# Performance work log

Hardware: AMD Instinct MI355X
Metric: run time of the kernel (lower is better)

## Reference

```python
import jax, jax.numpy as jnp
import numpy as np

D_MODEL = 1024
NUM_HEADS = 16
D_HEAD = D_MODEL // NUM_HEADS
THETA = 10000.0
NEG_INF = -1e9


def apply_rope(x, theta=THETA):
    # x: (..., S, Dh) with interleaved pairs (2i, 2i+1)
    S, Dh = x.shape[-2], x.shape[-1]
    inv_freq = 1.0 / (theta ** (jnp.arange(0, Dh, 2, dtype=jnp.float32) / Dh))  # (Dh/2,)
    ang = jnp.arange(S, dtype=jnp.float32)[:, None] * inv_freq[None, :]          # (S, Dh/2)
    cos, sin = jnp.cos(ang), jnp.sin(ang)
    x1 = x[..., 0::2]
    x2 = x[..., 1::2]
    r1 = x1 * cos - x2 * sin
    r2 = x1 * sin + x2 * cos
    # interleave back
    return jnp.stack([r1, r2], axis=-1).reshape(x.shape)


def setup_inputs() -> dict:
    key = jax.random.key(0)
    ks = jax.random.split(key, 5)
    B, S = 2, 2048
    scale = 1.0 / np.sqrt(D_MODEL)
    return {
        "x": jax.random.normal(ks[0], (B, S, D_MODEL), dtype=jnp.float32),
        "Wq": jax.random.normal(ks[1], (D_MODEL, D_MODEL), dtype=jnp.float32) * scale,
        "Wk": jax.random.normal(ks[2], (D_MODEL, D_MODEL), dtype=jnp.float32) * scale,
        "Wv": jax.random.normal(ks[3], (D_MODEL, D_MODEL), dtype=jnp.float32) * scale,
        "Wo": jax.random.normal(ks[4], (D_MODEL, D_MODEL), dtype=jnp.float32) * scale,
    }


def reference(x, Wq, Wk, Wv, Wo):
    B, S, _ = x.shape
    def split_heads(t):
        return t.reshape(B, S, NUM_HEADS, D_HEAD).transpose(0, 2, 1, 3)  # (B,H,S,Dh)
    # nn.Linear(bias=False): y = x @ W.T
    Q = split_heads(x @ Wq.T)
    K = split_heads(x @ Wk.T)
    V = split_heads(x @ Wv.T)
    Q = apply_rope(Q)
    K = apply_rope(K)
    scale = 1.0 / jnp.sqrt(jnp.asarray(D_HEAD, dtype=x.dtype))
    scores = jnp.einsum("bhqd,bhkd->bhqk", Q, K) * scale  # (B,H,S,S)
    causal = jnp.tril(jnp.ones((S, S), dtype=bool))
    scores = jnp.where(causal, scores, NEG_INF)
    attn = jax.nn.softmax(scores, axis=-1)
    out = jnp.einsum("bhqk,bhkd->bhqd", attn, V)
    out = out.transpose(0, 2, 1, 3).reshape(B, S, D_MODEL)
    return out @ Wo.T
```

## Files before the change

### kernel.cpp

```cpp
#include <hip/hip_runtime.h>
#include <hip/hip_bf16.h>
#include <stdint.h>

typedef __attribute__((ext_vector_type(8))) short bf8;
typedef __attribute__((ext_vector_type(4))) float f4;

#define MFMA16(a, b, c) __builtin_amdgcn_mfma_f32_16x16x32_bf16((a), (b), (c), 0, 0, 0)

static __device__ __forceinline__ short f2b(float f) {
  uint32_t x = __float_as_uint(f);
  x += 0x7fffu + ((x >> 16) & 1u);
  return (short)(x >> 16);
}

static __device__ __forceinline__ uint32_t pk2(float a, float b) {
  return ((__float_as_uint(a) + 0x8000u) >> 16) |
         ((__float_as_uint(b) + 0x8000u) & 0xffff0000u);
}

static __device__ __forceinline__ void gload16(const short* g, void* l) {
  __builtin_amdgcn_global_load_lds(
      (const __attribute__((address_space(1))) void*)g,
      (__attribute__((address_space(3))) void*)l, 16, 0, 0);
}

__global__ void rope_kernel(float2* __restrict__ tab) {
  const int t = blockIdx.x * 256 + threadIdx.x;
  const int s = t >> 5, i = t & 31;
  const float inv = powf(10000.0f, -(float)i * (1.0f / 32.0f));
  const float ang = (float)s * inv;
  float sv, cv;
  sincosf(ang, &sv, &cv);
  tab[t] = make_float2(cv, sv);
}

__global__ void convert_kernel(const float* __restrict__ x,
                               const float* __restrict__ wq, const float* __restrict__ wk,
                               const float* __restrict__ wv, const float* __restrict__ wo,
                               short* __restrict__ xb, short* __restrict__ Wb) {
  const size_t i = ((size_t)blockIdx.x * 256 + threadIdx.x) * 8;
  const float* __restrict__ src;
  short* __restrict__ dst;
  if (i < 4194304u) {
    src = x + i;
    dst = xb + i;
  } else {
    const size_t j = i - 4194304u;
    const int z = (int)(j >> 20);
    const size_t o = j & 1048575u;
    src = (z == 0 ? wq : z == 1 ? wk : z == 2 ? wv : wo) + o;
    dst = Wb + j;
  }
  const float4 a = *(const float4*)src;
  const float4 b = *(const float4*)(src + 4);
  bf8 v;
  v[0] = f2b(a.x); v[1] = f2b(a.y); v[2] = f2b(a.z); v[3] = f2b(a.w);
  v[4] = f2b(b.x); v[5] = f2b(b.y); v[6] = f2b(b.z); v[7] = f2b(b.w);
  *(bf8*)dst = v;
}

template <int MODE>
__launch_bounds__(256, 2)
__global__ void gemm_kernel(const short* __restrict__ Ab, const short* __restrict__ Wb,
                            short* __restrict__ Qo, short* __restrict__ Ko,
                            short* __restrict__ VTo, float* __restrict__ Fo,
                            const float2* __restrict__ rope) {
  constexpr int K = 1024;
  const int bm = blockIdx.x, bn = blockIdx.y;
  const int z = (MODE == 0) ? blockIdx.z : 3;
  const short* __restrict__ Bb = Wb + ((size_t)z << 20);

  __shared__ short As[128 * 64];
  __shared__ short Bs[128 * 64];

  const int tid = threadIdx.x;
  const int lane = tid & 63;
  const int wave = tid >> 6;
  const int wr = wave >> 1, wc = wave & 1;
  const int lg = lane >> 4, lr = lane & 15;

  f4 acc[4][4];
#pragma unroll
  for (int i = 0; i < 4; i++)
#pragma unroll
    for (int j = 0; j < 4; j++) {
      acc[i][j][0] = 0.f; acc[i][j][1] = 0.f;
      acc[i][j][2] = 0.f; acc[i][j][3] = 0.f;
    }

  const int kc = tid & 7;
  const int srow = tid >> 3;
  const int kcs = (kc ^ (srow & 7)) * 8;
  char* const Asw = (char*)As + wave * 1024;
  char* const Bsw = (char*)Bs + wave * 1024;

  for (int k0 = 0; k0 < K; k0 += 64) {
#pragma unroll
    for (int i = 0; i < 4; i++) {
      const int row = srow + i * 32;
      gload16(Ab + (size_t)(bm * 128 + row) * K + k0 + kcs, Asw + i * 4096);
      gload16(Bb + (size_t)(bn * 128 + row) * K + k0 + kcs, Bsw + i * 4096);
    }
    __syncthreads();
#pragma unroll
    for (int kk = 0; kk < 2; kk++) {
      bf8 af[4], bb[4];
#pragma unroll
      for (int mi = 0; mi < 4; mi++) {
        const int row = wr * 64 + mi * 16 + lr;
        const int lb = (row * 128 + kk * 64 + lg * 16) ^ ((row & 7) << 4);
        af[mi] = *(const bf8*)((const char*)As + lb);
      }
#pragma unroll
      for (int ni = 0; ni < 4; ni++) {
        const int row = wc * 64 + ni * 16 + lr;
        const int lb = (row * 128 + kk * 64 + lg * 16) ^ ((row & 7) << 4);
        bb[ni] = *(const bf8*)((const char*)Bs + lb);
      }
#pragma unroll
      for (int mi = 0; mi < 4; mi++)
#pragma unroll
        for (int ni = 0; ni < 4; ni++)
          acc[mi][ni] = MFMA16(af[mi], bb[ni], acc[mi][ni]);
    }
    __syncthreads();
  }

  if (MODE == 1) {
#pragma unroll
    for (int mi = 0; mi < 4; mi++) {
      const int m0 = bm * 128 + wr * 64 + mi * 16 + lg * 4;
#pragma unroll
      for (int ni = 0; ni < 4; ni++) {
        const int n = bn * 128 + wc * 64 + ni * 16 + lr;
#pragma unroll
        for (int r = 0; r < 4; r++)
          Fo[(size_t)(m0 + r) * 1024 + n] = acc[mi][ni][r];
      }
    }
    return;
  }

  if (z == 2) {
#pragma unroll
    for (int mi = 0; mi < 4; mi++) {
      const int m0 = bm * 128 + wr * 64 + mi * 16 + lg * 4;
      const int b = m0 >> 11, s0 = m0 & 2047;
#pragma unroll
      for (int ni = 0; ni < 4; ni++) {
        const int n = bn * 128 + wc * 64 + ni * 16 + lr;
        ushort4 pk;
        pk.x = (unsigned short)f2b(acc[mi][ni][0]);
        pk.y = (unsigned short)f2b(acc[mi][ni][1]);
        pk.z = (unsigned short)f2b(acc[mi][ni][2]);
        pk.w = (unsigned short)f2b(acc[mi][ni][3]);
        *(ushort4*)(VTo + ((size_t)((b * 16 + (n >> 6)) * 64 + (n & 63))) * 2048 + s0) = pk;
      }
    }
  } else {
    short* __restrict__ Out = (z == 0) ? Qo : Ko;
    const float qscale = (z == 0) ? 0.18033688011112042f : 1.0f;
#pragma unroll
    for (int mi = 0; mi < 4; mi++) {
      const int m0 = bm * 128 + wr * 64 + mi * 16 + lg * 4;
      const int b = m0 >> 11, s0 = m0 & 2047;
#pragma unroll
      for (int ni = 0; ni < 4; ni++) {
        const int n = bn * 128 + wc * 64 + ni * 16 + lr;
        const int h = n >> 6, d = n & 63;
        const float sgn = (d & 1) ? 1.0f : -1.0f;
#pragma unroll
        for (int r = 0; r < 4; r++) {
          const float v = acc[mi][ni][r];
          const float p = __shfl_xor(v, 1);
          const float2 cs = rope[((s0 + r) << 5) + (d >> 1)];
          const float res = (v * cs.x + sgn * p * cs.y) * qscale;
          Out[((size_t)(b * 16 + h) * 2048 + (s0 + r)) * 64 + d] = f2b(res);
        }
      }
    }
  }
}

__launch_bounds__(256, 2)
__global__ void attn_kernel(const short* __restrict__ Qg, const short* __restrict__ Kg,
                            const short* __restrict__ Vg, short* __restrict__ AO) {
  const int S = 2048;
  const int id = blockIdx.x;
  const int xcd = id & 7, r = id >> 3;
  const int bh = xcd * 4 + (r & 3);
  const int i = r >> 2;
  const int tid = threadIdx.x;
  const int lane = tid & 63, wave = tid >> 6;
  const int lg = lane >> 4, lr = lane & 15;
  const short* __restrict__ Qp = Qg + (size_t)bh * S * 64;
  const short* __restrict__ Kp = Kg + (size_t)bh * S * 64;
  const short* __restrict__ Vp = Vg + (size_t)bh * 64 * S;

  __shared__ short KB[2][64 * 64];
  __shared__ short VB[2][64 * 64];
  __shared__ short PB[4][2][16 * 64];

  const int tL = 16 * wave + i;
  const int tH = 127 - tL;
  const int qbaseT[2] = {tH << 4, tL << 4};
  const int nkvT[2] = {(16 * tH + 79) >> 6, (16 * tL + 79) >> 6};
  const int blk_nkv = (2111 - 16 * i) >> 6;

  const int rsub = lane >> 3;
  const int chsw = ((lane & 7) ^ rsub) * 8;
  const int row0 = (2 * wave) * 8 + rsub;
  const int row1 = (2 * wave + 1) * 8 + rsub;
  char* const kd0 = (char*)nullptr;

#define STAGE_KV(buf, kvb_)                                                        \
  do {                                                                             \
    gload16(Kp + (size_t)((kvb_) + row0) * 64 + chsw, (char*)KB[buf] + (2 * wave) * 1024);     \
    gload16(Kp + (size_t)((kvb_) + row1) * 64 + chsw, (char*)KB[buf] + (2 * wave + 1) * 1024); \
    gload16(Vp + (size_t)row0 * 2048 + (kvb_) + chsw, (char*)VB[buf] + (2 * wave) * 1024);     \
    gload16(Vp + (size_t)row1 * 2048 + (kvb_) + chsw, (char*)VB[buf] + (2 * wave + 1) * 1024); \
  } while (0)

  bf8 qf[2][2];
#pragma unroll
  for (int tt = 0; tt < 2; tt++)
#pragma unroll
    for (int ks = 0; ks < 2; ks++)
      qf[tt][ks] = *(const bf8*)(Qp + (size_t)(qbaseT[tt] + lr) * 64 + ks * 32 + lg * 8);

  f4 o[2][4];
#pragma unroll
  for (int tt = 0; tt < 2; tt++)
#pragma unroll
    for (int dt = 0; dt < 4; dt++) {
      o[tt][dt][0] = 0.f; o[tt][dt][1] = 0.f; o[tt][dt][2] = 0.f; o[tt][dt][3] = 0.f;
    }
  float mrun[2] = {-1e30f, -1e30f};
  float lsum[2] = {0.f, 0.f};

  char* const PwT[2] = {(char*)&PB[wave][0][0], (char*)&PB[wave][1][0]};
  const int rowoff = lr * 128;
  const int sw = (lr & 7) << 4;

  STAGE_KV(0, 0);
  __syncthreads();

  for (int kb = 0; kb < blk_nkv; kb++) {
    const int kvb = kb * 64;
    const int cur = kb & 1;

    if (kb + 1 < blk_nkv) STAGE_KV(cur ^ 1, kvb + 64);

    if (kb < nkvT[0]) {
      const char* Kc = (const char*)KB[cur];
      const char* Vc = (const char*)VB[cur];

      bf8 kf[4][2];
#pragma unroll
      for (int nt = 0; nt < 4; nt++) {
        const int row = nt * 16 + lr;
        const int base = row * 128 + lg * 16;
        const int rsw = (row & 7) << 4;
        kf[nt][0] = *(const bf8*)(Kc + (base ^ rsw));
        kf[nt][1] = *(const bf8*)(Kc + ((base + 64) ^ rsw));
      }

      asm volatile("s_waitcnt lgkmcnt(0)" ::: "memory");

#pragma unroll
      for (int tt = 0; tt < 2; tt++) {
        if (kb < nkvT[tt]) {
          f4 st[4];
          __builtin_amdgcn_s_setprio(1);
#pragma unroll
          for (int nt = 0; nt < 4; nt++) {
            f4 c;
            c[0] = 0.f; c[1] = 0.f; c[2] = 0.f; c[3] = 0.f;
            c = MFMA16(kf[nt][0], qf[tt][0], c);
            c = MFMA16(kf[nt][1], qf[tt][1], c);
            st[nt] = c;
          }
          __builtin_amdgcn_s_setprio(0);

          if ((kvb + 63) > qbaseT[tt]) {
            const int q = qbaseT[tt] + lr;
#pragma unroll
            for (int nt = 0; nt < 4; nt++)
#pragma unroll
              for (int rr = 0; rr < 4; rr++) {
                const int kv = kvb + nt * 16 + lg * 4 + rr;
                if (kv > q) st[nt][rr] = -1e9f;
              }
          }

          float m0 = fmaxf(fmaxf(st[0][0], st[0][1]), fmaxf(st[0][2], st[0][3]));
#pragma unroll
          for (int nt = 1; nt < 4; nt++)
            m0 = fmaxf(m0, fmaxf(fmaxf(st[nt][0], st[nt][1]), fmaxf(st[nt][2], st[nt][3])));
          m0 = fmaxf(m0, __shfl_xor(m0, 16));
          m0 = fmaxf(m0, __shfl_xor(m0, 32));

          if (__any(m0 - mrun[tt] > 8.0f)) {
            const float mn = fmaxf(mrun[tt], m0);
            const float corr = __builtin_amdgcn_exp2f(mrun[tt] - mn);
            mrun[tt] = mn;
            lsum[tt] *= corr;
#pragma unroll
            for (int rr = 0; rr < 4; rr++) {
              const float co = __shfl(corr, (lg << 2) + rr);
#pragma unroll
              for (int dt = 0; dt < 4; dt++) o[tt][dt][rr] *= co;
            }
          }

#pragma unroll
          for (int nt = 0; nt < 4; nt++) {
            const float p0 = __builtin_amdgcn_exp2f(st[nt][0] - mrun[tt]);
            const float p1 = __builtin_amdgcn_exp2f(st[nt][1] - mrun[tt]);
            const float p2 = __builtin_amdgcn_exp2f(st[nt][2] - mrun[tt]);
            const float p3 = __builtin_amdgcn_exp2f(st[nt][3] - mrun[tt]);
            lsum[tt] += (p0 + p1) + (p2 + p3);
            *(uint2*)(PwT[tt] + ((rowoff + nt * 32 + lg * 8) ^ sw)) =
                make_uint2(pk2(p0, p1), pk2(p2, p3));
          }
        }
      }

      asm volatile("s_waitcnt lgkmcnt(0)" ::: "memory");

      bf8 vf[4][2];
#pragma unroll
      for (int dt = 0; dt < 4; dt++) {
        const int row = dt * 16 + lr;
        const int base = row * 128 + lg * 16;
        const int rsw = (row & 7) << 4;
        vf[dt][0] = *(const bf8*)(Vc + (base ^ rsw));
        vf[dt][1] = *(const bf8*)(Vc + ((base + 64) ^ rsw));
      }

#pragma unroll
      for (int tt = 0; tt < 2; tt++) {
        if (kb < nkvT[tt]) {
          bf8 pf[2];
#pragma unroll
          for (int ks = 0; ks < 2; ks++)
            pf[ks] = *(const bf8*)(PwT[tt] + ((rowoff + ks * 64 + lg * 16) ^ sw));
          __builtin_amdgcn_s_setprio(1);
#pragma unroll
          for (int dt = 0; dt < 4; dt++) {
            o[tt][dt] = MFMA16(pf[0], vf[dt][0], o[tt][dt]);
            o[tt][dt] = MFMA16(pf[1], vf[dt][1], o[tt][dt]);
          }
          __builtin_amdgcn_s_setprio(0);
        }
      }
    }

    __syncthreads();
  }

  const int b = bh >> 4, h = bh & 15;
#pragma unroll
  for (int tt = 0; tt < 2; tt++) {
    float s = lsum[tt];
    s += __shfl_xor(s, 16);
    s += __shfl_xor(s, 32);
    const float inv = 1.0f / s;
    float inv_o[4];
#pragma unroll
    for (int rr = 0; rr < 4; rr++) inv_o[rr] = __shfl(inv, (lg << 2) + rr);
#pragma unroll
    for (int rr = 0; rr < 4; rr++) {
      const int q = qbaseT[tt] + lg * 4 + rr;
#pragma unroll
      for (int dt = 0; dt < 4; dt++) {
        const int d = dt * 16 + lr;
        AO[((size_t)b * 2048 + q) * 1024 + h * 64 + d] = f2b(o[tt][dt][rr] * inv_o[rr]);
      }
    }
  }
#undef STAGE_KV
}

extern "C" void kernel_launch(void* const* d_in, const int* in_sizes, int n_in,
                              void* d_out, int out_size, void* d_ws, size_t ws_size,
                              hipStream_t stream) {
  const float* x  = (const float*)d_in[0];
  const float* wq = (const float*)d_in[1];
  const float* wk = (const float*)d_in[2];
  const float* wv = (const float*)d_in[3];
  const float* wo = (const float*)d_in[4];
  float* out = (float*)d_out;

  char* ws = (char*)d_ws;
  short*  Qb  = (short*)(ws);
  short*  Kb  = (short*)(ws + (8ull  << 20));
  short*  VTb = (short*)(ws + (16ull << 20));
  short*  AOb = (short*)(ws + (24ull << 20));
  short*  xb  = AOb;
  short*  Wb  = (short*)(ws + (32ull << 20));
  float2* tab = (float2*)(ws + (40ull << 20));

  convert_kernel<<<4096, 256, 0, stream>>>(x, wq, wk, wv, wo, xb, Wb);
  rope_kernel<<<256, 256, 0, stream>>>(tab);
  gemm_kernel<0><<<dim3(32, 8, 3), 256, 0, stream>>>(
      xb, Wb, Qb, Kb, VTb, nullptr, tab);
  attn_kernel<<<512, 256, 0, stream>>>(Qb, Kb, VTb, AOb);
  gemm_kernel<1><<<dim3(32, 8, 1), 256, 0, stream>>>(
      AOb, Wb, nullptr, nullptr, nullptr, out, nullptr);
}
```

Measured before the change: 117.3 us.

## Split long causal query tiles across two KV segments and merge partial results

```diff
diff --git a/kernel.cpp b/kernel.cpp
--- a/kernel.cpp
+++ b/kernel.cpp
@@ -11,6 +11,10 @@
   uint32_t x = __float_as_uint(f);
   x += 0x7fffu + ((x >> 16) & 1u);
   return (short)(x >> 16);
+}
+
+static __device__ __forceinline__ float b2f(short v) {
+  return __uint_as_float(((uint32_t)(uint16_t)v) << 16);
 }
 
 static __device__ __forceinline__ uint32_t pk2(float a, float b) {
@@ -182,14 +186,19 @@
   }
 }
 
-__launch_bounds__(256, 2)
+__launch_bounds__(256, 4)
 __global__ void attn_kernel(const short* __restrict__ Qg, const short* __restrict__ Kg,
-                            const short* __restrict__ Vg, short* __restrict__ AO) {
+                            const short* __restrict__ Vg, short* __restrict__ AO,
+                            short* __restrict__ PO1, float* __restrict__ PM,
+                            float* __restrict__ PL) {
   const int S = 2048;
   const int id = blockIdx.x;
-  const int xcd = id & 7, r = id >> 3;
-  const int bh = xcd * 4 + (r & 3);
-  const int i = r >> 2;
+  const int xcd = id & 7;
+  const int rest = id >> 3;
+  const int bh = xcd * 4 + (rest & 3);
+  const int rem = rest >> 2;
+  const int seg = rem & 1;
+  const int i = rem >> 1;
   const int tid = threadIdx.x;
   const int lane = tid & 63, wave = tid >> 6;
   const int lg = lane >> 4, lr = lane & 15;
@@ -199,19 +208,20 @@
 
   __shared__ short KB[2][64 * 64];
   __shared__ short VB[2][64 * 64];
-  __shared__ short PB[4][2][16 * 64];
-
-  const int tL = 16 * wave + i;
+  __shared__ short PB[4][16 * 64];
+
+  const int tL = 4 * i + wave;
   const int tH = 127 - tL;
   const int qbaseT[2] = {tH << 4, tL << 4};
-  const int nkvT[2] = {(16 * tH + 79) >> 6, (16 * tL + 79) >> 6};
-  const int blk_nkv = (2111 - 16 * i) >> 6;
+  const int nkvL = i + 1;
+  const int nkvH = 32 - i;
+  const int k0 = seg ? 16 : 0;
+  const int kend = seg ? nkvH : 16;
 
   const int rsub = lane >> 3;
   const int chsw = ((lane & 7) ^ rsub) * 8;
   const int row0 = (2 * wave) * 8 + rsub;
   const int row1 = (2 * wave + 1) * 8 + rsub;
-  char* const kd0 = (char*)nullptr;
 
 #define STAGE_KV(buf, kvb_)                                                        \
   do {                                                                             \
@@ -223,10 +233,13 @@
 
   bf8 qf[2][2];
 #pragma unroll
-  for (int tt = 0; tt < 2; tt++)
+  for (int ks = 0; ks < 2; ks++)
+    qf[0][ks] = *(const bf8*)(Qp + (size_t)(qbaseT[0] + lr) * 64 + ks * 32 + lg * 8);
+  if (seg == 0) {
 #pragma unroll
     for (int ks = 0; ks < 2; ks++)
-      qf[tt][ks] = *(const bf8*)(Qp + (size_t)(qbaseT[tt] + lr) * 64 + ks * 32 + lg * 8);
+      qf[1][ks] = *(const bf8*)(Qp + (size_t)(qbaseT[1] + lr) * 64 + ks * 32 + lg * 8);
+  }
 
   f4 o[2][4];
 #pragma unroll
@@ -238,131 +251,147 @@
   float mrun[2] = {-1e30f, -1e30f};
   float lsum[2] = {0.f, 0.f};
 
-  char* const PwT[2] = {(char*)&PB[wave][0][0], (char*)&PB[wave][1][0]};
+  char* const Pw = (char*)&PB[wave][0];
   const int rowoff = lr * 128;
   const int sw = (lr & 7) << 4;
 
-  STAGE_KV(0, 0);
+  STAGE_KV(0, k0 * 64);
   __syncthreads();
 
-  for (int kb = 0; kb < blk_nkv; kb++) {
+  for (int kb = k0; kb < kend; kb++) {
     const int kvb = kb * 64;
-    const int cur = kb & 1;
-
-    if (kb + 1 < blk_nkv) STAGE_KV(cur ^ 1, kvb + 64);
-
-    if (kb < nkvT[0]) {
-      const char* Kc = (const char*)KB[cur];
-      const char* Vc = (const char*)VB[cur];
-
-      bf8 kf[4][2];
+    const int cur = (kb - k0) & 1;
+
+    if (kb + 1 < kend) STAGE_KV(cur ^ 1, kvb + 64);
+
+    const char* Kc = (const char*)KB[cur];
+    const char* Vc = (const char*)VB[cur];
+
+    bf8 kf[4][2], vf[4][2];
+#pragma unroll
+    for (int nt = 0; nt < 4; nt++) {
+      const int row = nt * 16 + lr;
+      const int base = row * 128 + lg * 16;
+      const int rsw = (row & 7) << 4;
+      kf[nt][0] = *(const bf8*)(Kc + (base ^ rsw));
+      kf[nt][1] = *(const bf8*)(Kc + ((base + 64) ^ rsw));
+      vf[nt][0] = *(const bf8*)(Vc + (base ^ rsw));
+      vf[nt][1] = *(const bf8*)(Vc + ((base + 64) ^ rsw));
+    }
+
+#pragma unroll
+    for (int tt = 0; tt < 2; tt++) {
+      if (tt == 1 && (seg != 0 || kb >= nkvL)) continue;
+
+      f4 st[4];
+      __builtin_amdgcn_s_setprio(1);
 #pragma unroll
       for (int nt = 0; nt < 4; nt++) {
-        const int row = nt * 16 + lr;
-        const int base = row * 128 + lg * 16;
-        const int rsw = (row & 7) << 4;
-        kf[nt][0] = *(const bf8*)(Kc + (base ^ rsw));
-        kf[nt][1] = *(const bf8*)(Kc + ((base + 64) ^ rsw));
+        f4 c;
+        c[0] = 0.f; c[1] = 0.f; c[2] = 0.f; c[3] = 0.f;
+        c = MFMA16(kf[nt][0], qf[tt][0], c);
+        c = MFMA16(kf[nt][1], qf[tt][1], c);
+        st[nt] = c;
+      }
+      __builtin_amdgcn_s_setprio(0);
+
+      if ((kvb + 63) > qbaseT[tt]) {
+        const int q = qbaseT[tt] + lr;
+#pragma unroll
+        for (int nt = 0; nt < 4; nt++)
+#pragma unroll
+          for (int rr = 0; rr < 4; rr++) {
+            const int kv = kvb + nt * 16 + lg * 4 + rr;
+            if (kv > q) st[nt][rr] = -1e9f;
+          }
+      }
+
+      float m0 = fmaxf(fmaxf(st[0][0], st[0][1]), fmaxf(st[0][2], st[0][3]));
+#pragma unroll
+      for (int nt = 1; nt < 4; nt++)
+        m0 = fmaxf(m0, fmaxf(fmaxf(st[nt][0], st[nt][1]), fmaxf(st[nt][2], st[nt][3])));
+      m0 = fmaxf(m0, __shfl_xor(m0, 16));
+      m0 = fmaxf(m0, __shfl_xor(m0, 32));
+
+      if (__any(m0 - mrun[tt] > 8.0f)) {
+        const float mn = fmaxf(mrun[tt], m0);
+        const float corr = __builtin_amdgcn_exp2f(mrun[tt] - mn);
+        mrun[tt] = mn;
+        lsum[tt] *= corr;
+#pragma unroll
+        for (int rr = 0; rr < 4; rr++) {
+          const float co = __shfl(corr, (lg << 2) + rr);
+#pragma unroll
+          for (int dt = 0; dt < 4; dt++) o[tt][dt][rr] *= co;
+        }
       }
 
       asm volatile("s_waitcnt lgkmcnt(0)" ::: "memory");
 
 #pragma unroll
-      for (int tt = 0; tt < 2; tt++) {
-        if (kb < nkvT[tt]) {
-          f4 st[4];
-          __builtin_amdgcn_s_setprio(1);
-#pragma unroll
-          for (int nt = 0; nt < 4; nt++) {
-            f4 c;
-            c[0] = 0.f; c[1] = 0.f; c[2] = 0.f; c[3] = 0.f;
-            c = MFMA16(kf[nt][0], qf[tt][0], c);
-            c = MFMA16(kf[nt][1], qf[tt][1], c);
-            st[nt] = c;
-          }
-          __builtin_amdgcn_s_setprio(0);
-
-          if ((kvb + 63) > qbaseT[tt]) {
-            const int q = qbaseT[tt] + lr;
-#pragma unroll
-            for (int nt = 0; nt < 4; nt++)
-#pragma unroll
-              for (int rr = 0; rr < 4; rr++) {
-                const int kv = kvb + nt * 16 + lg * 4 + rr;
-                if (kv > q) st[nt][rr] = -1e9f;
-              }
-          }
-
-          float m0 = fmaxf(fmaxf(st[0][0], st[0][1]), fmaxf(st[0][2], st[0][3]));
-#pragma unroll
-          for (int nt = 1; nt < 4; nt++)
-            m0 = fmaxf(m0, fmaxf(fmaxf(st[nt][0], st[nt][1]), fmaxf(st[nt][2], st[nt][3])));
-          m0 = fmaxf(m0, __shfl_xor(m0, 16));
-          m0 = fmaxf(m0, __shfl_xor(m0, 32));
-
-          if (__any(m0 - mrun[tt] > 8.0f)) {
-            const float mn = fmaxf(mrun[tt], m0);
-            const float corr = __builtin_amdgcn_exp2f(mrun[tt] - mn);
-            mrun[tt] = mn;
-            lsum[tt] *= corr;
-#pragma unroll
-            for (int rr = 0; rr < 4; rr++) {
-              const float co = __shfl(corr, (lg << 2) + rr);
-#pragma unroll
-              for (int dt = 0; dt < 4; dt++) o[tt][dt][rr] *= co;
-            }
-          }
-
-#pragma unroll
-          for (int nt = 0; nt < 4; nt++) {
-            const float p0 = __builtin_amdgcn_exp2f(st[nt][0] - mrun[tt]);
-            const float p1 = __builtin_amdgcn_exp2f(st[nt][1] - mrun[tt]);
-            const float p2 = __builtin_amdgcn_exp2f(st[nt][2] - mrun[tt]);
-            const float p3 = __builtin_amdgcn_exp2f(st[nt][3] - mrun[tt]);
-            lsum[tt] += (p0 + p1) + (p2 + p3);
-            *(uint2*)(PwT[tt] + ((rowoff + nt * 32 + lg * 8) ^ sw)) =
-                make_uint2(pk2(p0, p1), pk2(p2, p3));
-          }
+      for (int nt = 0; nt < 4; nt++) {
+        const float p0 = __builtin_amdgcn_exp2f(st[nt][0] - mrun[tt]);
+        const float p1 = __builtin_amdgcn_exp2f(st[nt][1] - mrun[tt]);
+        const float p2 = __builtin_amdgcn_exp2f(st[nt][2] - mrun[tt]);
+        const float p3 = __builtin_amdgcn_exp2f(st[nt][3] - mrun[tt]);
+        lsum[tt] += (p0 + p1) + (p2 + p3);
+        *(uint2*)(Pw + ((rowoff + nt * 32 + lg * 8) ^ sw)) =
+            make_uint2(pk2(p0, p1), pk2(p2, p3));
+      }
+
+      asm volatile("s_waitcnt lgkmcnt(0)" ::: "memory");
+
+      bf8 pf[2];
+#pragma unroll
+      for (int ks = 0; ks < 2; ks++)
+        pf[ks] = *(const bf8*)(Pw + ((rowoff + ks * 64 + lg * 16) ^ sw));
+
+      __builtin_amdgcn_s_setprio(1);
+#pragma unroll
+      for (int dt = 0; dt < 4; dt++) {
+        o[tt][dt] = MFMA16(pf[0], vf[dt][0], o[tt][dt]);
+        o[tt][dt] = MFMA16(pf[1], vf[dt][1], o[tt][dt]);
+      }
+      __builtin_amdgcn_s_setprio(0);
+    }
+
+    __syncthreads();
+  }
+
+  const int b = bh >> 4, h = bh & 15;
+  const int pt = bh * 64 + (tH - 64);
+
+  {
+    float s = lsum[0];
+    s += __shfl_xor(s, 16);
+    s += __shfl_xor(s, 32);
+    if (lg == 0) {
+      PM[(seg * 2048 + pt) * 16 + lr] = mrun[0];
+      PL[(seg * 2048 + pt) * 16 + lr] = s;
+    }
+    const float inv = 1.0f / s;
+    float inv_o[4];
+#pragma unroll
+    for (int rr = 0; rr < 4; rr++) inv_o[rr] = __shfl(inv, (lg << 2) + rr);
+#pragma unroll
+    for (int rr = 0; rr < 4; rr++) {
+      const int row = lg * 4 + rr;
+#pragma unroll
+      for (int dt = 0; dt < 4; dt++) {
+        const int d = dt * 16 + lr;
+        const short v = f2b(o[0][dt][rr] * inv_o[rr]);
+        if (seg == 0) {
+          const int q = qbaseT[0] + row;
+          AO[((size_t)b * 2048 + q) * 1024 + h * 64 + d] = v;
+        } else {
+          PO1[((size_t)pt * 16 + row) * 64 + d] = v;
         }
       }
-
-      asm volatile("s_waitcnt lgkmcnt(0)" ::: "memory");
-
-      bf8 vf[4][2];
-#pragma unroll
-      for (int dt = 0; dt < 4; dt++) {
-        const int row = dt * 16 + lr;
-        const int base = row * 128 + lg * 16;
-        const int rsw = (row & 7) << 4;
-        vf[dt][0] = *(const bf8*)(Vc + (base ^ rsw));
-        vf[dt][1] = *(const bf8*)(Vc + ((base + 64) ^ rsw));
-      }
-
-#pragma unroll
-      for (int tt = 0; tt < 2; tt++) {
-        if (kb < nkvT[tt]) {
-          bf8 pf[2];
-#pragma unroll
-          for (int ks = 0; ks < 2; ks++)
-            pf[ks] = *(const bf8*)(PwT[tt] + ((rowoff + ks * 64 + lg * 16) ^ sw));
-          __builtin_amdgcn_s_setprio(1);
-#pragma unroll
-          for (int dt = 0; dt < 4; dt++) {
-            o[tt][dt] = MFMA16(pf[0], vf[dt][0], o[tt][dt]);
-            o[tt][dt] = MFMA16(pf[1], vf[dt][1], o[tt][dt]);
-          }
-          __builtin_amdgcn_s_setprio(0);
-        }
-      }
-    }
-
-    __syncthreads();
-  }
-
-  const int b = bh >> 4, h = bh & 15;
-#pragma unroll
-  for (int tt = 0; tt < 2; tt++) {
-    float s = lsum[tt];
+    }
+  }
+
+  if (seg == 0) {
+    float s = lsum[1];
     s += __shfl_xor(s, 16);
     s += __shfl_xor(s, 32);
     const float inv = 1.0f / s;
@@ -371,15 +400,39 @@
     for (int rr = 0; rr < 4; rr++) inv_o[rr] = __shfl(inv, (lg << 2) + rr);
 #pragma unroll
     for (int rr = 0; rr < 4; rr++) {
-      const int q = qbaseT[tt] + lg * 4 + rr;
+      const int q = qbaseT[1] + lg * 4 + rr;
 #pragma unroll
       for (int dt = 0; dt < 4; dt++) {
         const int d = dt * 16 + lr;
-        AO[((size_t)b * 2048 + q) * 1024 + h * 64 + d] = f2b(o[tt][dt][rr] * inv_o[rr]);
+        AO[((size_t)b * 2048 + q) * 1024 + h * 64 + d] = f2b(o[1][dt][rr] * inv_o[rr]);
       }
     }
   }
 #undef STAGE_KV
+}
+
+__global__ void merge_kernel(short* __restrict__ AO, const short* __restrict__ PO1,
+                             const float* __restrict__ PM, const float* __restrict__ PL) {
+  const int pt = blockIdx.x;
+  const int bh = pt >> 6, tH = 64 + (pt & 63);
+  const int b = bh >> 4, h = bh & 15;
+  const int d = threadIdx.x;
+#pragma unroll 4
+  for (int r = 0; r < 16; r++) {
+    const float m0 = PM[pt * 16 + r];
+    const float m1 = PM[(2048 + pt) * 16 + r];
+    const float l0 = PL[pt * 16 + r];
+    const float l1 = PL[(2048 + pt) * 16 + r];
+    const float m = fmaxf(m0, m1);
+    const float w0 = l0 * __builtin_amdgcn_exp2f(m0 - m);
+    const float w1 = l1 * __builtin_amdgcn_exp2f(m1 - m);
+    const float wi = 1.0f / (w0 + w1);
+    const int q = tH * 16 + r;
+    const size_t ao = ((size_t)b * 2048 + q) * 1024 + h * 64 + d;
+    const float o0 = b2f(AO[ao]);
+    const float o1 = b2f(PO1[((size_t)pt * 16 + r) * 64 + d]);
+    AO[ao] = f2b((o0 * w0 + o1 * w1) * wi);
+  }
 }
 
 extern "C" void kernel_launch(void* const* d_in, const int* in_sizes, int n_in,
@@ -400,12 +453,16 @@
   short*  xb  = AOb;
   short*  Wb  = (short*)(ws + (32ull << 20));
   float2* tab = (float2*)(ws + (40ull << 20));
+  short*  PO1 = (short*)(ws + (32ull << 20));
+  float*  PM  = (float*)(ws + (36ull << 20));
+  float*  PL  = (float*)(ws + (36ull << 20) + (1u << 18));
 
   convert_kernel<<<4096, 256, 0, stream>>>(x, wq, wk, wv, wo, xb, Wb);
   rope_kernel<<<256, 256, 0, stream>>>(tab);
   gemm_kernel<0><<<dim3(32, 8, 3), 256, 0, stream>>>(
       xb, Wb, Qb, Kb, VTb, nullptr, tab);
-  attn_kernel<<<512, 256, 0, stream>>>(Qb, Kb, VTb, AOb);
+  attn_kernel<<<1024, 256, 0, stream>>>(Qb, Kb, VTb, AOb, PO1, PM, PL);
+  merge_kernel<<<2048, 64, 0, stream>>>(AOb, PO1, PM, PL);
   gemm_kernel<1><<<dim3(32, 8, 1), 256, 0, stream>>>(
       AOb, Wb, nullptr, nullptr, nullptr, out, nullptr);
 }
```

After: 225.1 us. 1.92x slower.
